# Kernel tuning notes

Hardware: AMD Instinct MI355X
Metric: run time of the kernel (lower is better)

Reference implementation:

```python
import jax, jax.numpy as jnp
import numpy as np

V = 32000; D = 512; H = 8; DH = D // H; L = 12; E = 8; FF = 2048
B = 2; S = 1024; MAXPOS = 2048
EPS = 1e-6; NEG = -1e9


def _rmsnorm(x, w):
    return x * jax.lax.rsqrt(jnp.mean(x * x, axis=-1, keepdims=True) + EPS) * w


def setup_inputs() -> dict:
    key = jax.random.key(0)
    ks = jax.random.split(key, 10)
    s = 0.02
    n = lambda k, shp: jax.random.normal(k, shp, jnp.float32) * s
    return {
        "input_ids": jax.random.randint(ks[0], (B, S), 0, V),
        "tok_emb": n(ks[1], (V, D)),
        "pos_emb": n(ks[2], (MAXPOS, D)),
        "Wqkv": n(ks[3], (L, D, 3 * D)), "bqkv": jnp.zeros((L, 3 * D), jnp.float32),
        "Wo": n(ks[4], (L, D, D)), "bo": jnp.zeros((L, D), jnp.float32),
        "rW": n(ks[5], (L, D, E)), "rb": jnp.zeros((L, E), jnp.float32),
        "eW1": n(ks[6], (L, E, D, FF)), "eb1": jnp.zeros((L, E, FF), jnp.float32),
        "eW2": n(ks[7], (L, E, FF, D)), "eb2": jnp.zeros((L, E, D), jnp.float32),
        "n1w": jnp.ones((L, D), jnp.float32), "n2w": jnp.ones((L, D), jnp.float32),
        "now": jnp.ones((D,), jnp.float32), "lmW": n(ks[8], (D, V)),
    }


def _forward(input_ids, tok_emb, pos_emb, Wqkv, bqkv, Wo, bo, rW, rb,
             eW1, eb1, eW2, eb2, n1w, n2w, now, lmW):
    x = tok_emb[input_ids] + pos_emb[:S]              # [B,S,D]
    causal = jnp.tril(jnp.ones((S, S), bool))         # lower-triangular mask

    def step(x, p):
        wqkv, bq, wo, bo_, rw, rb_, w1, b1, w2, b2, g1, g2 = p
        # --- causal self-attention ---
        h = _rmsnorm(x, g1)
        qkv = h @ wqkv + bq
        q, k, v = [t.reshape(B, S, H, DH) for t in jnp.split(qkv, 3, axis=-1)]
        scores = jnp.einsum('bqhd,bkhd->bhqk', q, k) / jnp.sqrt(jnp.float32(DH))
        scores = jnp.where(causal, scores, NEG)
        attn = jax.nn.softmax(scores, axis=-1)
        o = jnp.einsum('bhqk,bkhd->bqhd', attn, v).reshape(B, S, D) @ wo + bo_
        x = x + o
        # --- MoE layer, top-1 routing ---
        h = _rmsnorm(x, g2)
        rl = h @ rw + rb_                              # router logits [B,S,E]
        probs = jax.nn.softmax(rl, axis=-1)
        top_w = jnp.max(probs, axis=-1)                # top-1 gate weight [B,S]
        top_i = jnp.argmax(probs, axis=-1)             # expert id [B,S]
        one_hot = jax.nn.one_hot(top_i, E, dtype=x.dtype)
        frac = jnp.mean(one_hot, axis=(0, 1))          # fraction of tokens per expert
        pmean = jnp.mean(probs, axis=(0, 1))           # mean router prob per expert
        aux = E * jnp.sum(frac * pmean)                # switch-style load-balance loss
        disp = (one_hot * top_w[..., None]).reshape(-1, E)   # [T,E] weighted dispatch
        hf = h.reshape(-1, D)                          # [T,D]
        hid = jax.nn.gelu(jnp.einsum('td,edf->etf', hf, w1) + b1[:, None, :], approximate=False)
        outs = jnp.einsum('etf,efd->etd', hid, w2) + b2[:, None, :]
        y = jnp.einsum('etd,te->td', outs, disp).reshape(B, S, D)  # scatter-combine
        x = x + y
        return x, (aux, rl)

    x, (auxes, rlogits) = jax.lax.scan(
        step, x, (Wqkv, bqkv, Wo, bo, rW, rb, eW1, eb1, eW2, eb2, n1w, n2w))
    logits = _rmsnorm(x, now) @ lmW                    # [B,S,V]
    return logits, jnp.sum(auxes), rlogits


def reference(input_ids, tok_emb, pos_emb, Wqkv, bqkv, Wo, bo, rW, rb,
              eW1, eb1, eW2, eb2, n1w, n2w, now, lmW):
    return _forward(input_ids, tok_emb, pos_emb, Wqkv, bqkv, Wo, bo, rW, rb,
                    eW1, eb1, eW2, eb2, n1w, n2w, now, lmW)
```

## Files before the change

### kernel.cpp

```cpp
#include <hip/hip_runtime.h>

constexpr int B_  = 2, S_ = 1024, T_ = 2048;
constexpr int D_  = 512, H_ = 8, DH_ = 64;
constexpr int L_  = 12, E_ = 8, FF_ = 2048;
constexpr int V_  = 32000, D3_ = 1536;

using half8_t = __attribute__((ext_vector_type(8))) _Float16;
using half2_t = __attribute__((ext_vector_type(2))) _Float16;
using f32x4_t = __attribute__((ext_vector_type(4))) float;

__device__ __forceinline__ float wred(float v){
#pragma unroll
  for (int off = 32; off; off >>= 1) v += __shfl_xor(v, off);
  return v;
}
__device__ __forceinline__ float gelu_f(float v){
  return 0.5f * v * (1.f + erff(v * 0.70710678118654752f));
}

__global__ void k_embed(const int* __restrict__ ids, const float* __restrict__ tok,
                        const float* __restrict__ pos, float* __restrict__ x){
  int t = blockIdx.x;
  int s = t & (S_ - 1);
  int id = ids[t];
  const float* tr = tok + (size_t)id * D_;
  const float* pr = pos + (size_t)s  * D_;
  float* xr = x + (size_t)t * D_;
  for (int d = threadIdx.x; d < D_; d += blockDim.x) xr[d] = tr[d] + pr[d];
}

__global__ __launch_bounds__(256) void k_rmsnorm(const float* __restrict__ x,
                                                 const float* __restrict__ w,
                                                 float* __restrict__ h){
  int t = blockIdx.x;
  const float* xr = x + (size_t)t * D_;
  float* hr = h + (size_t)t * D_;
  float ss = 0.f;
  for (int d = threadIdx.x; d < D_; d += 256){ float v = xr[d]; ss += v * v; }
  ss = wred(ss);
  __shared__ float sp[4];
  __shared__ float sscale;
  if ((threadIdx.x & 63) == 0) sp[threadIdx.x >> 6] = ss;
  __syncthreads();
  if (threadIdx.x == 0){
    float tot = sp[0] + sp[1] + sp[2] + sp[3];
    sscale = rsqrtf(tot / (float)D_ + 1e-6f);
  }
  __syncthreads();
  float sc = sscale;
  for (int d = threadIdx.x; d < D_; d += 256) hr[d] = xr[d] * sc * w[d];
}

__global__ __launch_bounds__(64) void k_norm_router(
    const float* __restrict__ x, const float* __restrict__ nw,
    const float* __restrict__ rW, const float* __restrict__ rb,
    float* __restrict__ h, float* __restrict__ rl_out,
    float* __restrict__ topw, int* __restrict__ topi){
  const int t = blockIdx.x, lane = threadIdx.x;
  const float* xr = x + (size_t)t * D_;
  const float4 xv0 = *reinterpret_cast<const float4*>(xr + (lane << 2));
  const float4 xv1 = *reinterpret_cast<const float4*>(xr + 256 + (lane << 2));
  float ss = xv0.x*xv0.x + xv0.y*xv0.y + xv0.z*xv0.z + xv0.w*xv0.w
           + xv1.x*xv1.x + xv1.y*xv1.y + xv1.z*xv1.z + xv1.w*xv1.w;
  ss = wred(ss);
  const float sc = rsqrtf(ss * (1.f / (float)D_) + 1e-6f);
  const float4 w0 = *reinterpret_cast<const float4*>(nw + (lane << 2));
  const float4 w1 = *reinterpret_cast<const float4*>(nw + 256 + (lane << 2));
  float hv[8];
  hv[0] = xv0.x*sc*w0.x; hv[1] = xv0.y*sc*w0.y; hv[2] = xv0.z*sc*w0.z; hv[3] = xv0.w*sc*w0.w;
  hv[4] = xv1.x*sc*w1.x; hv[5] = xv1.y*sc*w1.y; hv[6] = xv1.z*sc*w1.z; hv[7] = xv1.w*sc*w1.w;
  float* hr = h + (size_t)t * D_;
  *reinterpret_cast<float4*>(hr + (lane << 2))       = make_float4(hv[0], hv[1], hv[2], hv[3]);
  *reinterpret_cast<float4*>(hr + 256 + (lane << 2)) = make_float4(hv[4], hv[5], hv[6], hv[7]);
  float acc[8] = {0,0,0,0,0,0,0,0};
#pragma unroll
  for (int u = 0; u < 8; u++){
    const int d = (u < 4) ? ((lane << 2) + u) : (256 + (lane << 2) + u - 4);
    const float4 ra = *reinterpret_cast<const float4*>(rW + (size_t)d * E_);
    const float4 rb4 = *reinterpret_cast<const float4*>(rW + (size_t)d * E_ + 4);
    acc[0] += hv[u]*ra.x;  acc[1] += hv[u]*ra.y;  acc[2] += hv[u]*ra.z;  acc[3] += hv[u]*ra.w;
    acc[4] += hv[u]*rb4.x; acc[5] += hv[u]*rb4.y; acc[6] += hv[u]*rb4.z; acc[7] += hv[u]*rb4.w;
  }
  float rl[8];
#pragma unroll
  for (int e = 0; e < 8; e++) rl[e] = wred(acc[e]) + rb[e];
  float mx = rl[0];
#pragma unroll
  for (int e = 1; e < 8; e++) mx = fmaxf(mx, rl[e]);
  float p[8], s = 0.f;
#pragma unroll
  for (int e = 0; e < 8; e++){ p[e] = __expf(rl[e] - mx); s += p[e]; }
  const float inv = 1.f / s;
  int arg = 0; float best = rl[0];
#pragma unroll
  for (int e = 1; e < 8; e++) if (rl[e] > best){ best = rl[e]; arg = e; }
  if (lane == 0){
#pragma unroll
    for (int e = 0; e < 8; e++) rl_out[(size_t)t * E_ + e] = rl[e];
    topw[t] = p[arg] * inv;
    topi[t] = arg;
  }
}

__global__ __launch_bounds__(1024) void k_route_scan2(
    const int* __restrict__ topi, const float* __restrict__ rl,
    int* __restrict__ seg, int* __restrict__ perm, float* __restrict__ aux){
  __shared__ int cnt[8], segs[9], cur[8];
  __shared__ float psums[8];
  const int tid = threadIdx.x;
  if (tid < 8){ cnt[tid] = 0; psums[tid] = 0.f; }
  __syncthreads();
  const int t0 = tid, t1 = tid + 1024;
  const int e0 = topi[t0], e1 = topi[t1];
  atomicAdd(&cnt[e0], 1);
  atomicAdd(&cnt[e1], 1);
  float ps[8] = {0,0,0,0,0,0,0,0};
#pragma unroll
  for (int k = 0; k < 2; k++){
    const float* r = rl + (size_t)(k ? t1 : t0) * E_;
    float v[8];
#pragma unroll
    for (int e = 0; e < 8; e++) v[e] = r[e];
    float mx = v[0];
#pragma unroll
    for (int e = 1; e < 8; e++) mx = fmaxf(mx, v[e]);
    float s = 0.f;
#pragma unroll
    for (int e = 0; e < 8; e++){ v[e] = __expf(v[e] - mx); s += v[e]; }
    const float is = 1.f / s;
#pragma unroll
    for (int e = 0; e < 8; e++) ps[e] += v[e] * is;
  }
#pragma unroll
  for (int e = 0; e < 8; e++) ps[e] = wred(ps[e]);
  if ((tid & 63) == 0){
#pragma unroll
    for (int e = 0; e < 8; e++) atomicAdd(&psums[e], ps[e]);
  }
  __syncthreads();
  if (tid == 0){
    segs[0] = 0;
#pragma unroll
    for (int e = 0; e < 8; e++) segs[e + 1] = segs[e] + cnt[e];
#pragma unroll
    for (int e = 0; e < 8; e++) cur[e] = segs[e];
  }
  __syncthreads();
  if (tid < 9) seg[tid] = segs[tid];
  const int p0 = atomicAdd(&cur[e0], 1); perm[p0] = t0;
  const int p1 = atomicAdd(&cur[e1], 1); perm[p1] = t1;
  if (tid == 0){
    float av = 0.f;
#pragma unroll
    for (int e = 0; e < 8; e++) av += (float)cnt[e] * psums[e];
    aux[0] += 8.f * av * (1.f / ((float)T_ * (float)T_));
  }
}

template<int BM, int BN, int NPROD, int EPI, bool MOE, bool APERM, int SWZROWS>
__global__ __launch_bounds__(256) void k_mgemm(
    const float* __restrict__ A, const float* __restrict__ Bm,
    const float* __restrict__ bias, float* __restrict__ C,
    int M, int N, int K,
    const int* __restrict__ seg, const int* __restrict__ perm,
    const float* __restrict__ topw){
  constexpr int FM = BM / 32, FN = BN / 32;
  const int tid = threadIdx.x;
  int rowTile, colTile;
  if (SWZROWS > 0){
    const int nwg = gridDim.x;
    const int bid = blockIdx.x;
    const int lb = (bid & 7) * (nwg >> 3) + (bid >> 3);
    rowTile = lb % SWZROWS;
    colTile = lb / SWZROWS;
  } else {
    colTile = blockIdx.x; rowTile = blockIdx.y;
  }
  int e = 0, s0 = 0, cnt = M;
  if (MOE){ e = blockIdx.z; s0 = seg[e]; cnt = seg[e + 1] - s0; }
  const int row0 = rowTile * BM, col0 = colTile * BN;
  if (MOE && row0 >= cnt) return;
  const float* Bp = Bm + (size_t)e * K * N;
  const float* bp = bias + (size_t)e * N;

  __shared__ __align__(16) _Float16 Ah[BM * 32];
  __shared__ __align__(16) _Float16 Al[NPROD == 3 ? BM * 32 : 8];
  __shared__ __align__(16) _Float16 Bh[BN * 32];
  __shared__ __align__(16) _Float16 Bl[NPROD == 3 ? BN * 32 : 8];

  const int am = (BM == 64) ? (tid >> 2) : (tid >> 1);
  const int agrow = row0 + am;
  const bool aval = agrow < cnt;
  const float* Arow = nullptr;
  if (aval){
    int ridx = APERM ? perm[s0 + agrow] : (MOE ? s0 + agrow : agrow);
    Arow = A + (size_t)ridx * K;
  }
  const int asub = am >> 4;
  const int cb = (BN == 128) ? ((tid & 31) << 2) : ((tid & 15) << 2);
  const int p0 = (BN == 128) ? (tid >> 5) : (tid >> 4);
  constexpr int NBI = (BN == 128) ? 2 : 1;

  const int lane = tid & 63, w = tid >> 6;
  const int wm0 = (w >> 1) * (BM / 2), wn0 = (w & 1) * (BN / 2);

  f32x4_t acc_hh[FM][FN];
  f32x4_t acc_mx[NPROD == 3 ? FM : 1][NPROD == 3 ? FN : 1];
#pragma unroll
  for (int i = 0; i < FM; i++)
#pragma unroll
    for (int j = 0; j < FN; j++){
      acc_hh[i][j] = (f32x4_t){0.f, 0.f, 0.f, 0.f};
      if (NPROD == 3) acc_mx[i][j] = (f32x4_t){0.f, 0.f, 0.f, 0.f};
    }

  for (int k0 = 0; k0 < K; k0 += 32){
    if (BM == 64){
      const int kg = tid & 3;
      float4 av0 = make_float4(0,0,0,0), av1 = make_float4(0,0,0,0);
      if (aval){
        av0 = *reinterpret_cast<const float4*>(Arow + k0 + (kg << 3));
        av1 = *reinterpret_cast<const float4*>(Arow + k0 + (kg << 3) + 4);
      }
      const float a8[8] = {av0.x, av0.y, av0.z, av0.w, av1.x, av1.y, av1.z, av1.w};
      half8_t hi, lo;
#pragma unroll
      for (int u = 0; u < 8; u++){
        hi[u] = (_Float16)a8[u];
        if (NPROD == 3) lo[u] = (_Float16)((a8[u] - (float)hi[u]) * 2048.f);
      }
      const int lidx = (am & 15) + (kg << 4);
      const int base = asub * 512 + ((lidx ^ (asub & 7)) << 3);
      *reinterpret_cast<half8_t*>(&Ah[base]) = hi;
      if (NPROD == 3) *reinterpret_cast<half8_t*>(&Al[base]) = lo;
    } else {
      const int kgb = (tid & 1) << 1;
#pragma unroll
      for (int kq = 0; kq < 2; kq++){
        const int kg = kgb + kq;
        float4 av0 = make_float4(0,0,0,0), av1 = make_float4(0,0,0,0);
        if (aval){
          av0 = *reinterpret_cast<const float4*>(Arow + k0 + (kg << 3));
          av1 = *reinterpret_cast<const float4*>(Arow + k0 + (kg << 3) + 4);
        }
        const float a8[8] = {av0.x, av0.y, av0.z, av0.w, av1.x, av1.y, av1.z, av1.w};
        half8_t hi;
#pragma unroll
        for (int u = 0; u < 8; u++) hi[u] = (_Float16)a8[u];
        const int lidx = (am & 15) + (kg << 4);
        *reinterpret_cast<half8_t*>(&Ah[asub * 512 + ((lidx ^ (asub & 7)) << 3)]) = hi;
      }
    }
#pragma unroll
    for (int it = 0; it < NBI; it++){
      const int kk = ((BN == 128) ? (p0 + (it << 3)) : p0) << 1;
      const int kg = kk >> 3, e2 = kk & 7;
      const float4 b0 = *reinterpret_cast<const float4*>(Bp + (size_t)(k0 + kk) * N + col0 + cb);
      const float4 b1 = *reinterpret_cast<const float4*>(Bp + (size_t)(k0 + kk + 1) * N + col0 + cb);
      const float b0a[4] = {b0.x, b0.y, b0.z, b0.w};
      const float b1a[4] = {b1.x, b1.y, b1.z, b1.w};
#pragma unroll
      for (int j = 0; j < 4; j++){
        const int c = cb + j, sub = c >> 4;
        const int lidx = (c & 15) + (kg << 4);
        const int base = sub * 512 + ((lidx ^ (sub & 7)) << 3) + e2;
        _Float16 h0 = (_Float16)b0a[j], h1 = (_Float16)b1a[j];
        *reinterpret_cast<half2_t*>(&Bh[base]) = (half2_t){h0, h1};
        if (NPROD == 3){
          _Float16 l0 = (_Float16)((b0a[j] - (float)h0) * 2048.f);
          _Float16 l1 = (_Float16)((b1a[j] - (float)h1) * 2048.f);
          *reinterpret_cast<half2_t*>(&Bl[base]) = (half2_t){l0, l1};
        }
      }
    }
    __syncthreads();
    half8_t fAh[FM], fBh[FN];
    half8_t fAl[NPROD == 3 ? FM : 1], fBl[NPROD == 3 ? FN : 1];
#pragma unroll
    for (int fm = 0; fm < FM; fm++){
      const int s = (wm0 >> 4) + fm;
      const int ofs = s * 512 + ((lane ^ (s & 7)) << 3);
      fAh[fm] = *reinterpret_cast<const half8_t*>(&Ah[ofs]);
      if (NPROD == 3) fAl[fm] = *reinterpret_cast<const half8_t*>(&Al[ofs]);
    }
#pragma unroll
    for (int fn = 0; fn < FN; fn++){
      const int s = (wn0 >> 4) + fn;
      const int ofs = s * 512 + ((lane ^ (s & 7)) << 3);
      fBh[fn] = *reinterpret_cast<const half8_t*>(&Bh[ofs]);
      if (NPROD == 3) fBl[fn] = *reinterpret_cast<const half8_t*>(&Bl[ofs]);
    }
#pragma unroll
    for (int fm = 0; fm < FM; fm++)
#pragma unroll
      for (int fn = 0; fn < FN; fn++){
        acc_hh[fm][fn] = __builtin_amdgcn_mfma_f32_16x16x32_f16(
            fAh[fm], fBh[fn], acc_hh[fm][fn], 0, 0, 0);
        if (NPROD == 3){
          acc_mx[fm][fn] = __builtin_amdgcn_mfma_f32_16x16x32_f16(
              fAh[fm], fBl[fn], acc_mx[fm][fn], 0, 0, 0);
          acc_mx[fm][fn] = __builtin_amdgcn_mfma_f32_16x16x32_f16(
              fAl[fm], fBh[fn], acc_mx[fm][fn], 0, 0, 0);
        }
      }
    __syncthreads();
  }

  const int lr = lane & 15, kg4 = lane >> 4;
#pragma unroll
  for (int fm = 0; fm < FM; fm++){
#pragma unroll
    for (int reg = 0; reg < 4; reg++){
      const int grow = row0 + wm0 + fm * 16 + (kg4 << 2) + reg;
      if (grow >= cnt) continue;
      int trow = 0; float tw = 0.f;
      if (EPI == 3){ trow = perm[s0 + grow]; tw = topw[trow]; }
#pragma unroll
      for (int fn = 0; fn < FN; fn++){
        const int col = col0 + wn0 + fn * 16 + lr;
        float v = acc_hh[fm][fn][reg];
        if (NPROD == 3) v += acc_mx[fm][fn][reg] * (1.f / 2048.f);
        if (EPI == 0){
          C[(size_t)grow * N + col] = v + bp[col];
        } else if (EPI == 1){
          C[(size_t)grow * N + col] += v + bp[col];
        } else if (EPI == 2){
          C[(size_t)(s0 + grow) * N + col] = gelu_f(v + bp[col]);
        } else if (EPI == 3){
          C[(size_t)trow * N + col] += tw * (v + bp[col]);
        } else {
          C[(size_t)grow * N + col] = v;
        }
      }
    }
  }
}

__global__ __launch_bounds__(256) void k_attn4(const float* __restrict__ qkv,
                                               float* __restrict__ o){
  __shared__ __align__(16) _Float16 Khi[4096], Klo[4096], Vhi[4096], Vlo[4096];
  __shared__ __align__(16) float pbuf[4][16 * 68];
  const int tid = threadIdx.x, w = tid >> 6, lane = tid & 63;
  const int lr = lane & 15, g = lane >> 4;
  const int bid = blockIdx.x;
  const int qt = bid & 15, h = (bid >> 4) & 7, b = bid >> 7;
  const size_t bbase = (size_t)(b << 10) * D3_;
  const int hoff = h * 64;
  const int qg = (qt << 6) + (w << 4) + lr;

  half8_t qhi[2], qlo[2];
#pragma unroll
  for (int ks = 0; ks < 2; ks++){
    const float* qp = qkv + bbase + (size_t)qg * D3_ + hoff + ks * 32 + g * 8;
    const float4 f0 = *reinterpret_cast<const float4*>(qp);
    const float4 f1 = *reinterpret_cast<const float4*>(qp + 4);
    const float qa[8] = {f0.x, f0.y, f0.z, f0.w, f1.x, f1.y, f1.z, f1.w};
#pragma unroll
    for (int e = 0; e < 8; e++){
      const float v = qa[e] * 0.125f;
      const _Float16 hi = (_Float16)v;
      qhi[ks][e] = hi;
      qlo[ks][e] = (_Float16)((v - (float)hi) * 2048.f);
    }
  }

  float m = -1e30f, l = 0.f;
  f32x4_t oacc[4];
#pragma unroll
  for (int s = 0; s < 4; s++) oacc[s] = (f32x4_t){0.f, 0.f, 0.f, 0.f};

  const int kK = tid >> 2, quad = tid & 3;
  const int kp = tid >> 3, oct = tid & 7;
  const int ntiles = qt + 1;

  for (int kt = 0; kt < ntiles; kt++){
    const int j0 = kt << 6;
    __syncthreads();
    {
      const float* kr = qkv + bbase + (size_t)(j0 + kK) * D3_ + 512 + hoff + quad * 16;
      const float4 f0 = *reinterpret_cast<const float4*>(kr);
      const float4 f1 = *reinterpret_cast<const float4*>(kr + 4);
      const float4 f2 = *reinterpret_cast<const float4*>(kr + 8);
      const float4 f3 = *reinterpret_cast<const float4*>(kr + 12);
      const float ka[16] = {f0.x,f0.y,f0.z,f0.w, f1.x,f1.y,f1.z,f1.w,
                            f2.x,f2.y,f2.z,f2.w, f3.x,f3.y,f3.z,f3.w};
      const int ksd = quad >> 1;
#pragma unroll
      for (int ch = 0; ch < 2; ch++){
        const int kgd = ((quad << 1) + ch) & 3;
        const int base = ksd * 2048 + (kK >> 4) * 512 + (((kK & 15) + (kgd << 4)) << 3);
        half8_t hi, lo;
#pragma unroll
        for (int e = 0; e < 8; e++){
          const float v = ka[ch * 8 + e];
          const _Float16 hv = (_Float16)v;
          hi[e] = hv;
          lo[e] = (_Float16)((v - (float)hv) * 2048.f);
        }
        *reinterpret_cast<half8_t*>(&Khi[base]) = hi;
        *reinterpret_cast<half8_t*>(&Klo[base]) = lo;
      }
    }
    {
      const int k0 = kp << 1;
      const float* vr = qkv + bbase + (size_t)(j0 + k0) * D3_ + 1024 + hoff + oct * 8;
      const float4 a0 = *reinterpret_cast<const float4*>(vr);
      const float4 a1 = *reinterpret_cast<const float4*>(vr + 4);
      const float4 b0 = *reinterpret_cast<const float4*>(vr + D3_);
      const float4 b1 = *reinterpret_cast<const float4*>(vr + D3_ + 4);
      const float va[8] = {a0.x,a0.y,a0.z,a0.w, a1.x,a1.y,a1.z,a1.w};
      const float vb[8] = {b0.x,b0.y,b0.z,b0.w, b1.x,b1.y,b1.z,b1.w};
      const int ksk = kp >> 4, kgk = (kp >> 2) & 3, e0 = (kp & 3) << 1;
#pragma unroll
      for (int j = 0; j < 8; j++){
        const int d = oct * 8 + j;
        const int lidx = (d & 15) + (kgk << 4);
        const int sw = lidx ^ kgk ^ (ksk << 2);
        const int fa = ksk * 2048 + (d >> 4) * 512 + (sw << 3) + e0;
        const _Float16 h0 = (_Float16)va[j], h1 = (_Float16)vb[j];
        *reinterpret_cast<half2_t*>(&Vhi[fa]) = (half2_t){h0, h1};
        const _Float16 l0 = (_Float16)((va[j] - (float)h0) * 2048.f);
        const _Float16 l1 = (_Float16)((vb[j] - (float)h1) * 2048.f);
        *reinterpret_cast<half2_t*>(&Vlo[fa]) = (half2_t){l0, l1};
      }
    }
    __syncthreads();

    f32x4_t dfr[4];
#pragma unroll
    for (int s = 0; s < 4; s++){
      f32x4_t acc = (f32x4_t){0.f, 0.f, 0.f, 0.f};
      f32x4_t mix = (f32x4_t){0.f, 0.f, 0.f, 0.f};
#pragma unroll
      for (int ks = 0; ks < 2; ks++){
        const int base = ks * 2048 + s * 512 + lane * 8;
        const half8_t khi = *reinterpret_cast<const half8_t*>(&Khi[base]);
        const half8_t klo = *reinterpret_cast<const half8_t*>(&Klo[base]);
        acc = __builtin_amdgcn_mfma_f32_16x16x32_f16(khi, qhi[ks], acc, 0, 0, 0);
        mix = __builtin_amdgcn_mfma_f32_16x16x32_f16(khi, qlo[ks], mix, 0, 0, 0);
        mix = __builtin_amdgcn_mfma_f32_16x16x32_f16(klo, qhi[ks], mix, 0, 0, 0);
      }
#pragma unroll
      for (int r = 0; r < 4; r++) dfr[s][r] = acc[r] + mix[r] * (1.f / 2048.f);
    }
    if (kt == qt){
#pragma unroll
      for (int s = 0; s < 4; s++)
#pragma unroll
        for (int r = 0; r < 4; r++){
          const int keyg = j0 + (g << 2) + r + (s << 4);
          if (keyg > qg) dfr[s][r] = -1e30f;
        }
    }
    float mloc = dfr[0][0];
#pragma unroll
    for (int s = 0; s < 4; s++)
#pragma unroll
      for (int r = 0; r < 4; r++) mloc = fmaxf(mloc, dfr[s][r]);
    mloc = fmaxf(mloc, __shfl_xor(mloc, 16));
    mloc = fmaxf(mloc, __shfl_xor(mloc, 32));
    const float mn = fmaxf(m, mloc);
    const float cr = __expf(m - mn);
    float psum = 0.f;
#pragma unroll
    for (int s = 0; s < 4; s++)
#pragma unroll
      for (int r = 0; r < 4; r++){
        const float p = __expf(dfr[s][r] - mn);
        psum += p;
        pbuf[w][lr * 68 + (s << 4) + (g << 2) + r] = p;
      }
    psum += __shfl_xor(psum, 16);
    psum += __shfl_xor(psum, 32);
    l = l * cr + psum;
    m = mn;
#pragma unroll
    for (int s = 0; s < 4; s++)
#pragma unroll
      for (int r = 0; r < 4; r++) oacc[s][r] *= cr;

    half8_t phi[2], plo[2];
#pragma unroll
    for (int ks = 0; ks < 2; ks++){
      const float* pp = &pbuf[w][lr * 68 + ks * 32 + g * 8];
      const float4 p0 = *reinterpret_cast<const float4*>(pp);
      const float4 p1 = *reinterpret_cast<const float4*>(pp + 4);
      const float pa[8] = {p0.x,p0.y,p0.z,p0.w, p1.x,p1.y,p1.z,p1.w};
#pragma unroll
      for (int e = 0; e < 8; e++){
        const _Float16 hv = (_Float16)pa[e];
        phi[ks][e] = hv;
        plo[ks][e] = (_Float16)((pa[e] - (float)hv) * 2048.f);
      }
    }
#pragma unroll
    for (int s = 0; s < 4; s++){
      f32x4_t mix = (f32x4_t){0.f, 0.f, 0.f, 0.f};
#pragma unroll
      for (int ks = 0; ks < 2; ks++){
        const int sw = lane ^ g ^ (ks << 2);
        const int base = ks * 2048 + s * 512 + sw * 8;
        const half8_t vhi = *reinterpret_cast<const half8_t*>(&Vhi[base]);
        const half8_t vlo = *reinterpret_cast<const half8_t*>(&Vlo[base]);
        oacc[s] = __builtin_amdgcn_mfma_f32_16x16x32_f16(vhi, phi[ks], oacc[s], 0, 0, 0);
        mix = __builtin_amdgcn_mfma_f32_16x16x32_f16(vhi, plo[ks], mix, 0, 0, 0);
        mix = __builtin_amdgcn_mfma_f32_16x16x32_f16(vlo, phi[ks], mix, 0, 0, 0);
      }
#pragma unroll
      for (int r = 0; r < 4; r++) oacc[s][r] += mix[r] * (1.f / 2048.f);
    }
  }

  const float linv = 1.f / l;
  float* orow = o + (size_t)((b << 10) + qg) * D_ + hoff;
#pragma unroll
  for (int s = 0; s < 4; s++)
#pragma unroll
    for (int r = 0; r < 4; r++){
      const int d = (g << 2) + r + (s << 4);
      orow[d] = oacc[s][r] * linv;
    }
}

extern "C" void kernel_launch(void* const* d_in, const int* in_sizes, int n_in,
                              void* d_out, int out_size, void* d_ws, size_t ws_size,
                              hipStream_t stream){
  const int*   ids  = (const int*)  d_in[0];
  const float* tok  = (const float*)d_in[1];
  const float* pos  = (const float*)d_in[2];
  const float* Wqkv = (const float*)d_in[3];
  const float* bqkv = (const float*)d_in[4];
  const float* Wo   = (const float*)d_in[5];
  const float* bo   = (const float*)d_in[6];
  const float* rW   = (const float*)d_in[7];
  const float* rb   = (const float*)d_in[8];
  const float* eW1  = (const float*)d_in[9];
  const float* eb1  = (const float*)d_in[10];
  const float* eW2  = (const float*)d_in[11];
  const float* eb2  = (const float*)d_in[12];
  const float* n1w  = (const float*)d_in[13];
  const float* n2w  = (const float*)d_in[14];
  const float* noww = (const float*)d_in[15];
  const float* lmW  = (const float*)d_in[16];

  float* out    = (float*)d_out;
  float* logits = out;
  float* aux    = out + (size_t)T_ * V_;
  float* rlog   = aux + 1;

  float* ws = (float*)d_ws;
  size_t off = 0;
  float* x     = ws + off; off += (size_t)T_ * D_;
  float* h     = ws + off; off += (size_t)T_ * D_;
  float* qkv   = ws + off; off += (size_t)T_ * D3_;
  float* attno = ws + off; off += (size_t)T_ * D_;
  float* hid   = ws + off; off += (size_t)T_ * FF_;
  float* topw  = ws + off; off += T_;
  int* topi    = (int*)(ws + off); off += T_;
  int* perm    = (int*)(ws + off); off += T_;
  int* seg     = (int*)(ws + off); off += (E_ + 1);

  hipMemsetAsync(aux, 0, sizeof(float), stream);
  k_embed<<<T_, 256, 0, stream>>>(ids, tok, pos, x);

  for (int l = 0; l < L_; l++){
    k_rmsnorm<<<T_, 256, 0, stream>>>(x, n1w + (size_t)l * D_, h);
    k_mgemm<64, 128, 3, 0, false, false, 0><<<dim3(D3_ / 128, T_ / 64), 256, 0, stream>>>(
        h, Wqkv + (size_t)l * D_ * D3_, bqkv + (size_t)l * D3_, qkv,
        T_, D3_, D_, seg, perm, topw);
    k_attn4<<<B_ * H_ * (S_ / 64), 256, 0, stream>>>(qkv, attno);
    k_mgemm<64, 64, 3, 1, false, false, 0><<<dim3(D_ / 64, T_ / 64), 256, 0, stream>>>(
        attno, Wo + (size_t)l * D_ * D_, bo + (size_t)l * D_, x,
        T_, D_, D_, seg, perm, topw);
    k_norm_router<<<T_, 64, 0, stream>>>(x, n2w + (size_t)l * D_,
        rW + (size_t)l * D_ * E_, rb + (size_t)l * E_,
        h, rlog + (size_t)l * T_ * E_, topw, topi);
    k_route_scan2<<<1, 1024, 0, stream>>>(topi, rlog + (size_t)l * T_ * E_, seg, perm, aux);
    k_mgemm<64, 128, 3, 2, true, true, 0><<<dim3(FF_ / 128, T_ / 64, E_), 256, 0, stream>>>(
        h, eW1 + (size_t)l * E_ * D_ * FF_, eb1 + (size_t)l * E_ * FF_, hid,
        T_, FF_, D_, seg, perm, topw);
    k_mgemm<64, 64, 3, 3, true, false, 0><<<dim3(D_ / 64, T_ / 64, E_), 256, 0, stream>>>(
        hid, eW2 + (size_t)l * E_ * FF_ * D_, eb2 + (size_t)l * E_ * D_, x,
        T_, D_, FF_, seg, perm, topw);
  }

  k_rmsnorm<<<T_, 256, 0, stream>>>(x, noww, h);
  k_mgemm<128, 128, 1, 4, false, false, 16><<<(T_ / 128) * (V_ / 128), 256, 0, stream>>>(
      h, lmW, noww , logits, T_, V_, D_, seg, perm, topw);
}
```

Measured before the change: 3.152 ms.

## Fuse RMSNorm into GEMM prologue and split long causal attention tiles

Removes the standalone RMSNorm kernels by computing each row's sum of squares inside the GEMM prologue and scaling A on load, for both the QKV projection and the LM head. Attention is reworked to balance causal work: the late query tiles are split into two KV-range halves whose partial results go to workspace and are merged by a new combine kernel, giving 384 blocks of similar size. K/V global loads are also prefetched into registers one tile ahead. Costs are an extra read pass over A per GEMM block, redundant norm computation across column tiles, and an additional kernel launch with a workspace round-trip.

```diff
diff --git a/kernel.cpp b/kernel.cpp
--- a/kernel.cpp
+++ b/kernel.cpp
@@ -27,28 +27,6 @@
   const float* pr = pos + (size_t)s  * D_;
   float* xr = x + (size_t)t * D_;
   for (int d = threadIdx.x; d < D_; d += blockDim.x) xr[d] = tr[d] + pr[d];
-}
-
-__global__ __launch_bounds__(256) void k_rmsnorm(const float* __restrict__ x,
-                                                 const float* __restrict__ w,
-                                                 float* __restrict__ h){
-  int t = blockIdx.x;
-  const float* xr = x + (size_t)t * D_;
-  float* hr = h + (size_t)t * D_;
-  float ss = 0.f;
-  for (int d = threadIdx.x; d < D_; d += 256){ float v = xr[d]; ss += v * v; }
-  ss = wred(ss);
-  __shared__ float sp[4];
-  __shared__ float sscale;
-  if ((threadIdx.x & 63) == 0) sp[threadIdx.x >> 6] = ss;
-  __syncthreads();
-  if (threadIdx.x == 0){
-    float tot = sp[0] + sp[1] + sp[2] + sp[3];
-    sscale = rsqrtf(tot / (float)D_ + 1e-6f);
-  }
-  __syncthreads();
-  float sc = sscale;
-  for (int d = threadIdx.x; d < D_; d += 256) hr[d] = xr[d] * sc * w[d];
 }
 
 __global__ __launch_bounds__(64) void k_norm_router(
@@ -157,13 +135,13 @@
   }
 }
 
-template<int BM, int BN, int NPROD, int EPI, bool MOE, bool APERM, int SWZROWS>
+template<int BM, int BN, int NPROD, int EPI, bool MOE, bool APERM, int SWZROWS, bool ANORM>
 __global__ __launch_bounds__(256) void k_mgemm(
     const float* __restrict__ A, const float* __restrict__ Bm,
     const float* __restrict__ bias, float* __restrict__ C,
     int M, int N, int K,
     const int* __restrict__ seg, const int* __restrict__ perm,
-    const float* __restrict__ topw){
+    const float* __restrict__ topw, const float* __restrict__ nw){
   constexpr int FM = BM / 32, FN = BN / 32;
   const int tid = threadIdx.x;
   int rowTile, colTile;
@@ -204,6 +182,36 @@
   const int lane = tid & 63, w = tid >> 6;
   const int wm0 = (w >> 1) * (BM / 2), wn0 = (w & 1) * (BN / 2);
 
+  float ascale = 1.f;
+  if (ANORM){
+    float ss = 0.f;
+    if (BM == 64){
+      const int kg = tid & 3;
+      for (int k0 = 0; k0 < K; k0 += 32){
+        const float4 a0 = *reinterpret_cast<const float4*>(Arow + k0 + (kg << 3));
+        const float4 a1 = *reinterpret_cast<const float4*>(Arow + k0 + (kg << 3) + 4);
+        ss += a0.x*a0.x + a0.y*a0.y + a0.z*a0.z + a0.w*a0.w
+            + a1.x*a1.x + a1.y*a1.y + a1.z*a1.z + a1.w*a1.w;
+      }
+      ss += __shfl_xor(ss, 1);
+      ss += __shfl_xor(ss, 2);
+    } else {
+      const int kgb = (tid & 1) << 1;
+      for (int k0 = 0; k0 < K; k0 += 32){
+#pragma unroll
+        for (int kq = 0; kq < 2; kq++){
+          const int kg = kgb + kq;
+          const float4 a0 = *reinterpret_cast<const float4*>(Arow + k0 + (kg << 3));
+          const float4 a1 = *reinterpret_cast<const float4*>(Arow + k0 + (kg << 3) + 4);
+          ss += a0.x*a0.x + a0.y*a0.y + a0.z*a0.z + a0.w*a0.w
+              + a1.x*a1.x + a1.y*a1.y + a1.z*a1.z + a1.w*a1.w;
+        }
+      }
+      ss += __shfl_xor(ss, 1);
+    }
+    ascale = rsqrtf(ss * (1.f / (float)K) + 1e-6f);
+  }
+
   f32x4_t acc_hh[FM][FN];
   f32x4_t acc_mx[NPROD == 3 ? FM : 1][NPROD == 3 ? FN : 1];
 #pragma unroll
@@ -222,7 +230,14 @@
         av0 = *reinterpret_cast<const float4*>(Arow + k0 + (kg << 3));
         av1 = *reinterpret_cast<const float4*>(Arow + k0 + (kg << 3) + 4);
       }
-      const float a8[8] = {av0.x, av0.y, av0.z, av0.w, av1.x, av1.y, av1.z, av1.w};
+      float a8[8] = {av0.x, av0.y, av0.z, av0.w, av1.x, av1.y, av1.z, av1.w};
+      if (ANORM){
+        const float4 w0 = *reinterpret_cast<const float4*>(nw + k0 + (kg << 3));
+        const float4 w1 = *reinterpret_cast<const float4*>(nw + k0 + (kg << 3) + 4);
+        const float wn8[8] = {w0.x, w0.y, w0.z, w0.w, w1.x, w1.y, w1.z, w1.w};
+#pragma unroll
+        for (int u = 0; u < 8; u++) a8[u] *= ascale * wn8[u];
+      }
       half8_t hi, lo;
 #pragma unroll
       for (int u = 0; u < 8; u++){
@@ -243,7 +258,14 @@
           av0 = *reinterpret_cast<const float4*>(Arow + k0 + (kg << 3));
           av1 = *reinterpret_cast<const float4*>(Arow + k0 + (kg << 3) + 4);
         }
-        const float a8[8] = {av0.x, av0.y, av0.z, av0.w, av1.x, av1.y, av1.z, av1.w};
+        float a8[8] = {av0.x, av0.y, av0.z, av0.w, av1.x, av1.y, av1.z, av1.w};
+        if (ANORM){
+          const float4 w0 = *reinterpret_cast<const float4*>(nw + k0 + (kg << 3));
+          const float4 w1 = *reinterpret_cast<const float4*>(nw + k0 + (kg << 3) + 4);
+          const float wn8[8] = {w0.x, w0.y, w0.z, w0.w, w1.x, w1.y, w1.z, w1.w};
+#pragma unroll
+          for (int u = 0; u < 8; u++) a8[u] *= ascale * wn8[u];
+        }
         half8_t hi;
 #pragma unroll
         for (int u = 0; u < 8; u++) hi[u] = (_Float16)a8[u];
@@ -336,14 +358,20 @@
   }
 }
 
-__global__ __launch_bounds__(256) void k_attn4(const float* __restrict__ qkv,
-                                               float* __restrict__ o){
+__global__ __launch_bounds__(256) void k_attn5(const float* __restrict__ qkv,
+                                               float* __restrict__ o,
+                                               float* __restrict__ attp,
+                                               float* __restrict__ attml){
   __shared__ __align__(16) _Float16 Khi[4096], Klo[4096], Vhi[4096], Vlo[4096];
   __shared__ __align__(16) float pbuf[4][16 * 68];
   const int tid = threadIdx.x, w = tid >> 6, lane = tid & 63;
   const int lr = lane & 15, g = lane >> 4;
   const int bid = blockIdx.x;
-  const int qt = bid & 15, h = (bid >> 4) & 7, b = bid >> 7;
+  int bh, qt, kt0, kt1, mode;
+  if (bid < 128){        bh = bid >> 3;            qt = 8 + (bid & 7);  kt0 = 0; kt1 = 7;  mode = 1; }
+  else if (bid < 256){   const int j = bid - 128;  bh = j >> 3; qt = 7 - (j & 7);  kt0 = 0; kt1 = qt; mode = 0; }
+  else {                 const int j = bid - 256;  bh = j >> 3; qt = 15 - (j & 7); kt0 = 8; kt1 = qt; mode = 2; }
+  const int b = bh >> 3, h = bh & 7;
   const size_t bbase = (size_t)(b << 10) * D3_;
   const int hoff = h * 64;
   const int qg = (qt << 6) + (w << 4) + lr;
@@ -371,59 +399,68 @@
 
   const int kK = tid >> 2, quad = tid & 3;
   const int kp = tid >> 3, oct = tid & 7;
-  const int ntiles = qt + 1;
-
-  for (int kt = 0; kt < ntiles; kt++){
+
+  float ka[16], va[8], vb[8];
+  auto loadregs = [&](int kt){
+    const int j0 = kt << 6;
+    const float* kr = qkv + bbase + (size_t)(j0 + kK) * D3_ + 512 + hoff + quad * 16;
+    const float4 f0 = *reinterpret_cast<const float4*>(kr);
+    const float4 f1 = *reinterpret_cast<const float4*>(kr + 4);
+    const float4 f2 = *reinterpret_cast<const float4*>(kr + 8);
+    const float4 f3 = *reinterpret_cast<const float4*>(kr + 12);
+    ka[0]=f0.x; ka[1]=f0.y; ka[2]=f0.z; ka[3]=f0.w;
+    ka[4]=f1.x; ka[5]=f1.y; ka[6]=f1.z; ka[7]=f1.w;
+    ka[8]=f2.x; ka[9]=f2.y; ka[10]=f2.z; ka[11]=f2.w;
+    ka[12]=f3.x; ka[13]=f3.y; ka[14]=f3.z; ka[15]=f3.w;
+    const int k0v = kp << 1;
+    const float* vr = qkv + bbase + (size_t)(j0 + k0v) * D3_ + 1024 + hoff + oct * 8;
+    const float4 a0 = *reinterpret_cast<const float4*>(vr);
+    const float4 a1 = *reinterpret_cast<const float4*>(vr + 4);
+    const float4 b0 = *reinterpret_cast<const float4*>(vr + D3_);
+    const float4 b1 = *reinterpret_cast<const float4*>(vr + D3_ + 4);
+    va[0]=a0.x; va[1]=a0.y; va[2]=a0.z; va[3]=a0.w;
+    va[4]=a1.x; va[5]=a1.y; va[6]=a1.z; va[7]=a1.w;
+    vb[0]=b0.x; vb[1]=b0.y; vb[2]=b0.z; vb[3]=b0.w;
+    vb[4]=b1.x; vb[5]=b1.y; vb[6]=b1.z; vb[7]=b1.w;
+  };
+  auto writelds = [&](){
+    const int ksd = quad >> 1;
+#pragma unroll
+    for (int ch = 0; ch < 2; ch++){
+      const int kgd = ((quad << 1) + ch) & 3;
+      const int base = ksd * 2048 + (kK >> 4) * 512 + (((kK & 15) + (kgd << 4)) << 3);
+      half8_t hi, lo;
+#pragma unroll
+      for (int e = 0; e < 8; e++){
+        const float v = ka[ch * 8 + e];
+        const _Float16 hv = (_Float16)v;
+        hi[e] = hv;
+        lo[e] = (_Float16)((v - (float)hv) * 2048.f);
+      }
+      *reinterpret_cast<half8_t*>(&Khi[base]) = hi;
+      *reinterpret_cast<half8_t*>(&Klo[base]) = lo;
+    }
+    const int ksk = kp >> 4, kgk = (kp >> 2) & 3, e0 = (kp & 3) << 1;
+#pragma unroll
+    for (int j = 0; j < 8; j++){
+      const int d = oct * 8 + j;
+      const int lidx = (d & 15) + (kgk << 4);
+      const int sw = lidx ^ kgk ^ (ksk << 2);
+      const int fa = ksk * 2048 + (d >> 4) * 512 + (sw << 3) + e0;
+      const _Float16 h0 = (_Float16)va[j], h1 = (_Float16)vb[j];
+      *reinterpret_cast<half2_t*>(&Vhi[fa]) = (half2_t){h0, h1};
+      const _Float16 l0 = (_Float16)((va[j] - (float)h0) * 2048.f);
+      const _Float16 l1 = (_Float16)((vb[j] - (float)h1) * 2048.f);
+      *reinterpret_cast<half2_t*>(&Vlo[fa]) = (half2_t){l0, l1};
+    }
+  };
+
+  loadregs(kt0);
+  for (int kt = kt0; kt <= kt1; kt++){
     const int j0 = kt << 6;
     __syncthreads();
-    {
-      const float* kr = qkv + bbase + (size_t)(j0 + kK) * D3_ + 512 + hoff + quad * 16;
-      const float4 f0 = *reinterpret_cast<const float4*>(kr);
-      const float4 f1 = *reinterpret_cast<const float4*>(kr + 4);
-      const float4 f2 = *reinterpret_cast<const float4*>(kr + 8);
-      const float4 f3 = *reinterpret_cast<const float4*>(kr + 12);
-      const float ka[16] = {f0.x,f0.y,f0.z,f0.w, f1.x,f1.y,f1.z,f1.w,
-                            f2.x,f2.y,f2.z,f2.w, f3.x,f3.y,f3.z,f3.w};
-      const int ksd = quad >> 1;
-#pragma unroll
-      for (int ch = 0; ch < 2; ch++){
-        const int kgd = ((quad << 1) + ch) & 3;
-        const int base = ksd * 2048 + (kK >> 4) * 512 + (((kK & 15) + (kgd << 4)) << 3);
-        half8_t hi, lo;
-#pragma unroll
-        for (int e = 0; e < 8; e++){
-          const float v = ka[ch * 8 + e];
-          const _Float16 hv = (_Float16)v;
-          hi[e] = hv;
-          lo[e] = (_Float16)((v - (float)hv) * 2048.f);
-        }
-        *reinterpret_cast<half8_t*>(&Khi[base]) = hi;
-        *reinterpret_cast<half8_t*>(&Klo[base]) = lo;
-      }
-    }
-    {
-      const int k0 = kp << 1;
-      const float* vr = qkv + bbase + (size_t)(j0 + k0) * D3_ + 1024 + hoff + oct * 8;
-      const float4 a0 = *reinterpret_cast<const float4*>(vr);
-      const float4 a1 = *reinterpret_cast<const float4*>(vr + 4);
-      const float4 b0 = *reinterpret_cast<const float4*>(vr + D3_);
-      const float4 b1 = *reinterpret_cast<const float4*>(vr + D3_ + 4);
-      const float va[8] = {a0.x,a0.y,a0.z,a0.w, a1.x,a1.y,a1.z,a1.w};
-      const float vb[8] = {b0.x,b0.y,b0.z,b0.w, b1.x,b1.y,b1.z,b1.w};
-      const int ksk = kp >> 4, kgk = (kp >> 2) & 3, e0 = (kp & 3) << 1;
-#pragma unroll
-      for (int j = 0; j < 8; j++){
-        const int d = oct * 8 + j;
-        const int lidx = (d & 15) + (kgk << 4);
-        const int sw = lidx ^ kgk ^ (ksk << 2);
-        const int fa = ksk * 2048 + (d >> 4) * 512 + (sw << 3) + e0;
-        const _Float16 h0 = (_Float16)va[j], h1 = (_Float16)vb[j];
-        *reinterpret_cast<half2_t*>(&Vhi[fa]) = (half2_t){h0, h1};
-        const _Float16 l0 = (_Float16)((va[j] - (float)h0) * 2048.f);
-        const _Float16 l1 = (_Float16)((vb[j] - (float)h1) * 2048.f);
-        *reinterpret_cast<half2_t*>(&Vlo[fa]) = (half2_t){l0, l1};
-      }
-    }
+    writelds();
+    if (kt < kt1) loadregs(kt + 1);
     __syncthreads();
 
     f32x4_t dfr[4];
@@ -511,15 +548,62 @@
     }
   }
 
-  const float linv = 1.f / l;
-  float* orow = o + (size_t)((b << 10) + qg) * D_ + hoff;
-#pragma unroll
-  for (int s = 0; s < 4; s++)
-#pragma unroll
-    for (int r = 0; r < 4; r++){
-      const int d = (g << 2) + r + (s << 4);
-      orow[d] = oacc[s][r] * linv;
-    }
+  if (mode == 0){
+    const float linv = 1.f / l;
+    float* orow = o + (size_t)((b << 10) + qg) * D_ + hoff;
+#pragma unroll
+    for (int s = 0; s < 4; s++)
+#pragma unroll
+      for (int r = 0; r < 4; r++){
+        const int d = (g << 2) + r + (s << 4);
+        orow[d] = oacc[s][r] * linv;
+      }
+  } else {
+    const int pidx = (((bh << 3) + (qt - 8)) << 1) + (mode - 1);
+    float* pO = attp + (size_t)pidx * 4096;
+    const int qloc = (w << 4) + lr;
+#pragma unroll
+    for (int s = 0; s < 4; s++)
+#pragma unroll
+      for (int r = 0; r < 4; r++){
+        const int d = (g << 2) + r + (s << 4);
+        pO[qloc * 64 + d] = oacc[s][r];
+      }
+    if (g == 0){
+      attml[pidx * 128 + qloc]      = m;
+      attml[pidx * 128 + 64 + qloc] = l;
+    }
+  }
+}
+
+__global__ __launch_bounds__(256) void k_attn_comb(const float* __restrict__ attp,
+                                                   const float* __restrict__ attml,
+                                                   float* __restrict__ o){
+  const int bid = blockIdx.x;
+  const int bh = bid >> 3, i = bid & 7, qt = 8 + i;
+  const int b = bh >> 3, h = bh & 7;
+  const int pidx0 = ((bh << 3) + i) << 1;
+  const float* pA = attp + (size_t)pidx0 * 4096;
+  const float* pB = pA + 4096;
+  const float* mlA = attml + pidx0 * 128;
+  const float* mlB = mlA + 128;
+  const int tid = threadIdx.x;
+  const int q = tid >> 2, dg = (tid & 3) << 4;
+  const float mA = mlA[q], lA = mlA[64 + q];
+  const float mB = mlB[q], lB = mlB[64 + q];
+  const float M = fmaxf(mA, mB);
+  const float cA = __expf(mA - M), cB = __expf(mB - M);
+  const float linv = 1.f / (lA * cA + lB * cB);
+  float* orow = o + (size_t)((b << 10) + (qt << 6) + q) * D_ + h * 64;
+#pragma unroll
+  for (int j = 0; j < 4; j++){
+    const int d = dg + (j << 2);
+    const float4 a = *reinterpret_cast<const float4*>(pA + q * 64 + d);
+    const float4 bb = *reinterpret_cast<const float4*>(pB + q * 64 + d);
+    *reinterpret_cast<float4*>(orow + d) = make_float4(
+        (a.x * cA + bb.x * cB) * linv, (a.y * cA + bb.y * cB) * linv,
+        (a.z * cA + bb.z * cB) * linv, (a.w * cA + bb.w * cB) * linv);
+  }
 }
 
 extern "C" void kernel_launch(void* const* d_in, const int* in_sizes, int n_in,
@@ -559,32 +643,33 @@
   int* topi    = (int*)(ws + off); off += T_;
   int* perm    = (int*)(ws + off); off += T_;
   int* seg     = (int*)(ws + off); off += (E_ + 1);
+  float* attp  = ws + off; off += 16 * 8 * 2 * 4096;
+  float* attml = ws + off; off += 16 * 8 * 2 * 128;
 
   hipMemsetAsync(aux, 0, sizeof(float), stream);
   k_embed<<<T_, 256, 0, stream>>>(ids, tok, pos, x);
 
   for (int l = 0; l < L_; l++){
-    k_rmsnorm<<<T_, 256, 0, stream>>>(x, n1w + (size_t)l * D_, h);
-    k_mgemm<64, 128, 3, 0, false, false, 0><<<dim3(D3_ / 128, T_ / 64), 256, 0, stream>>>(
-        h, Wqkv + (size_t)l * D_ * D3_, bqkv + (size_t)l * D3_, qkv,
-        T_, D3_, D_, seg, perm, topw);
-    k_attn4<<<B_ * H_ * (S_ / 64), 256, 0, stream>>>(qkv, attno);
-    k_mgemm<64, 64, 3, 1, false, false, 0><<<dim3(D_ / 64, T_ / 64), 256, 0, stream>>>(
+    k_mgemm<64, 128, 3, 0, false, false, 0, true><<<dim3(D3_ / 128, T_ / 64), 256, 0, stream>>>(
+        x, Wqkv + (size_t)l * D_ * D3_, bqkv + (size_t)l * D3_, qkv,
+        T_, D3_, D_, seg, perm, topw, n1w + (size_t)l * D_);
+    k_attn5<<<384, 256, 0, stream>>>(qkv, attno, attp, attml);
+    k_attn_comb<<<128, 256, 0, stream>>>(attp, attml, attno);
+    k_mgemm<64, 64, 3, 1, false, false, 0, false><<<dim3(D_ / 64, T_ / 64), 256, 0, stream>>>(
         attno, Wo + (size_t)l * D_ * D_, bo + (size_t)l * D_, x,
-        T_, D_, D_, seg, perm, topw);
+        T_, D_, D_, seg, perm, topw, nullptr);
     k_norm_router<<<T_, 64, 0, stream>>>(x, n2w + (size_t)l * D_,
         rW + (size_t)l * D_ * E_, rb + (size_t)l * E_,
         h, rlog + (size_t)l * T_ * E_, topw, topi);
     k_route_scan2<<<1, 1024, 0, stream>>>(topi, rlog + (size_t)l * T_ * E_, seg, perm, aux);
-    k_mgemm<64, 128, 3, 2, true, true, 0><<<dim3(FF_ / 128, T_ / 64, E_), 256, 0, stream>>>(
+    k_mgemm<64, 128, 3, 2, true, true, 0, false><<<dim3(FF_ / 128, T_ / 64, E_), 256, 0, stream>>>(
         h, eW1 + (size_t)l * E_ * D_ * FF_, eb1 + (size_t)l * E_ * FF_, hid,
-        T_, FF_, D_, seg, perm, topw);
-    k_mgemm<64, 64, 3, 3, true, false, 0><<<dim3(D_ / 64, T_ / 64, E_), 256, 0, stream>>>(
+        T_, FF_, D_, seg, perm, topw, nullptr);
+    k_mgemm<64, 64, 3, 3, true, false, 0, false><<<dim3(D_ / 64, T_ / 64, E_), 256, 0, stream>>>(
         hid, eW2 + (size_t)l * E_ * FF_ * D_, eb2 + (size_t)l * E_ * D_, x,
-        T_, D_, FF_, seg, perm, topw);
-  }
-
-  k_rmsnorm<<<T_, 256, 0, stream>>>(x, noww, h);
-  k_mgemm<128, 128, 1, 4, false, false, 16><<<(T_ / 128) * (V_ / 128), 256, 0, stream>>>(
-      h, lmW, noww , logits, T_, V_, D_, seg, perm, topw);
-}
+        T_, D_, FF_, seg, perm, topw, nullptr);
+  }
+
+  k_mgemm<128, 128, 1, 4, false, false, 16, true><<<(T_ / 128) * (V_ / 128), 256, 0, stream>>>(
+      x, lmW, nullptr, logits, T_, V_, D_, seg, perm, topw, noww);
+}
```

Result: no change. 3.164 ms (+0.4%).
